# Kernel tuning notes

Hardware: AMD Instinct MI355X
Metric: run time of the kernel (lower is better)

## Reference

```python
import jax, jax.numpy as jnp
import numpy as np

N = 50000      # nodes
E = 1600000    # edges (before self loops)
IN = 128
OUT = 128
H = 4
HD = OUT // H  # head dim = 32


def setup_inputs() -> dict:
    key = jax.random.key(0)
    k1, k2, k3, k4, k5 = jax.random.split(key, 5)
    x = jax.random.normal(k1, (N, IN), dtype=jnp.float32)
    edge_index = jax.random.randint(k2, (2, E), 0, N, dtype=jnp.int64)
    # xavier-uniform-ish scales
    W = jax.random.normal(k3, (OUT, IN), dtype=jnp.float32) * (1.0 / np.sqrt(IN))
    att_src = jax.random.normal(k4, (1, H, HD), dtype=jnp.float32) * 0.1
    att_dst = jax.random.normal(k5, (1, H, HD), dtype=jnp.float32) * 0.1
    return {"x": x, "edge_index": edge_index, "W": W, "att_src": att_src, "att_dst": att_dst}


def reference(x, edge_index, W, att_src, att_dst):
    n = x.shape[0]
    # add self loops (tg.utils.add_self_loops appends [i, i] edges)
    loops = jnp.arange(n, dtype=edge_index.dtype)
    ei = jnp.concatenate([edge_index, jnp.stack([loops, loops])], axis=1)
    src, dst = ei[0], ei[1]

    # linear projection, split into heads: [n, H, HD]
    h = (x @ W.T).reshape(n, H, HD)

    # per-node attention logits per head: [n, H]
    a_src = jnp.sum(h * att_src, axis=-1)
    a_dst = jnp.sum(h * att_dst, axis=-1)

    # per-edge attention score: gather + leaky_relu
    alpha = a_src[src] + a_dst[dst]                      # [Etot, H]
    alpha = jax.nn.leaky_relu(alpha, negative_slope=0.2)

    # segment softmax grouped by destination node (numerically stable)
    m = jax.ops.segment_max(alpha, dst, num_segments=n)  # [n, H]
    e = jnp.exp(alpha - m[dst])
    s = jax.ops.segment_sum(e, dst, num_segments=n)      # [n, H]
    e = e / s[dst]                                       # [Etot, H]

    # weighted scatter-add aggregation; f_additive adds 1 to the weights
    msg = h[src] * (e[:, :, None] + 1.0)                 # [Etot, H, HD]
    out = jax.ops.segment_sum(msg, dst, num_segments=n)  # [n, H, HD]
    return out.reshape(n, -1)
```

## Files before the change

kernel.cpp:

```cpp
#include <hip/hip_runtime.h>

#define N_NODES 50000
#define E_EDGES 1600000
#define ETOT    (E_EDGES + N_NODES)
#define DIN  128
#define DOUT 128
#define NH   4
#define HD   32

typedef unsigned short ushort_t;
typedef unsigned int uint_t;
typedef __attribute__((ext_vector_type(8))) short bfrag;
typedef __attribute__((ext_vector_type(4))) float ffrag;

__device__ __forceinline__ ushort_t f2bf(float f) {
  uint_t u = __float_as_uint(f);
  u += 0x7fffu + ((u >> 16) & 1u);
  return (ushort_t)(u >> 16);
}
__device__ __forceinline__ float bf_lo(uint_t u) {
  return __uint_as_float(u << 16);
}
__device__ __forceinline__ float bf_hi(uint_t u) {
  return __uint_as_float(u & 0xffff0000u);
}

#define BSZ   256
#define NBUCK ((N_NODES + BSZ - 1) / BSZ)
#define CAP   10240
#define EPB_A 8192
#define NBLK_A ((ETOT + EPB_A - 1) / EPB_A)
#define NCHUNK 13

__global__ __launch_bounds__(256, 4) void fused_binA_gemm_kernel(
    const int* __restrict__ ei, int* __restrict__ gcur,
    uint_t* __restrict__ ebuf,
    const float* __restrict__ x, const float* __restrict__ W,
    const float* __restrict__ att_src, const float* __restrict__ att_dst,
    ushort_t* __restrict__ hb, float* __restrict__ a_src,
    float* __restrict__ a_dst) {
  __shared__ int hist[NBUCK];
  __shared__ int base[NBUCK];
  __shared__ ushort_t Ws[DIN * DOUT];
  const int tid = threadIdx.x;

  if (blockIdx.x < NBLK_A) {
    const int e0 = blockIdx.x * EPB_A;
    const int e1 = min(e0 + EPB_A, ETOT);
    for (int i = tid; i < NBUCK; i += 256) hist[i] = 0;
    __syncthreads();
    for (int e = e0 + tid; e < e1; e += 256) {
      int di = (e < E_EDGES) ? ei[E_EDGES + e] : (e - E_EDGES);
      atomicAdd(&hist[di >> 8], 1);
    }
    __syncthreads();
    for (int i = tid; i < NBUCK; i += 256) {
      int c = hist[i];
      base[i] = (c > 0) ? (i * CAP + atomicAdd(&gcur[i], c)) : 0;
      hist[i] = 0;
    }
    __syncthreads();
    for (int e = e0 + tid; e < e1; e += 256) {
      int si, di;
      if (e < E_EDGES) { si = ei[e]; di = ei[E_EDGES + e]; }
      else             { si = e - E_EDGES; di = si; }
      int b = di >> 8;
      int pos = base[b] + atomicAdd(&hist[b], 1);
      if (pos < (b + 1) * CAP)
        ebuf[pos] = ((uint_t)(di & 255) << 24) | (uint_t)si;
    }
    return;
  }

  const int gb = blockIdx.x - NBLK_A;
  for (int u = tid; u < 2048; u += 256) {
    int row = u >> 4;
    float4 w0 = *(const float4*)&W[u * 8];
    float4 w1 = *(const float4*)&W[u * 8 + 4];
    uint4 pk;
    pk.x = (uint_t)f2bf(w0.x) | ((uint_t)f2bf(w0.y) << 16);
    pk.y = (uint_t)f2bf(w0.z) | ((uint_t)f2bf(w0.w) << 16);
    pk.z = (uint_t)f2bf(w1.x) | ((uint_t)f2bf(w1.y) << 16);
    pk.w = (uint_t)f2bf(w1.z) | ((uint_t)f2bf(w1.w) << 16);
    *(uint4*)&Ws[(u ^ (row & 7)) * 8] = pk;
  }
  __syncthreads();

  const int wv = tid >> 6, l = tid & 63;
  const int lr = l & 15, lg = l >> 4;
  const int nbase = gb * 64 + wv * 16;
  int na = nbase + lr;
  if (na >= N_NODES) na = N_NODES - 1;
  const float* xrow = x + (size_t)na * DIN;

  ffrag acc[8];
#pragma unroll
  for (int oc = 0; oc < 8; oc++) acc[oc] = (ffrag){0.f, 0.f, 0.f, 0.f};

#pragma unroll
  for (int kt = 0; kt < 4; kt++) {
    float4 x0 = *(const float4*)&xrow[kt * 32 + lg * 8];
    float4 x1 = *(const float4*)&xrow[kt * 32 + lg * 8 + 4];
    bfrag a;
    a[0] = (short)f2bf(x0.x); a[1] = (short)f2bf(x0.y);
    a[2] = (short)f2bf(x0.z); a[3] = (short)f2bf(x0.w);
    a[4] = (short)f2bf(x1.x); a[5] = (short)f2bf(x1.y);
    a[6] = (short)f2bf(x1.z); a[7] = (short)f2bf(x1.w);
#pragma unroll
    for (int oc = 0; oc < 8; oc++) {
      const int u = ((oc * 16 + lr) << 4) + kt * 4 + lg;
      const bfrag b = *(const bfrag*)&Ws[(u ^ (lr & 7)) * 8];
      acc[oc] = __builtin_amdgcn_mfma_f32_16x16x32_bf16(a, b, acc[oc], 0, 0, 0);
    }
  }

#pragma unroll
  for (int oc = 0; oc < 8; oc++) {
#pragma unroll
    for (int j = 0; j < 4; j++) {
      int n = nbase + lg * 4 + j;
      if (n < N_NODES)
        hb[((size_t)n << 7) + oc * 16 + lr] = f2bf(acc[oc][j]);
    }
  }

  float asv[8], adv[8];
#pragma unroll
  for (int oc = 0; oc < 8; oc++) {
    asv[oc] = att_src[oc * 16 + lr];
    adv[oc] = att_dst[oc * 16 + lr];
  }
#pragma unroll
  for (int j = 0; j < 4; j++) {
    float ps[4] = {0.f, 0.f, 0.f, 0.f};
    float pd[4] = {0.f, 0.f, 0.f, 0.f};
#pragma unroll
    for (int oc = 0; oc < 8; oc++) {
      ps[oc >> 1] = fmaf(acc[oc][j], asv[oc], ps[oc >> 1]);
      pd[oc >> 1] = fmaf(acc[oc][j], adv[oc], pd[oc >> 1]);
    }
#pragma unroll
    for (int off = 1; off < 16; off <<= 1) {
#pragma unroll
      for (int hd = 0; hd < 4; hd++) {
        ps[hd] += __shfl_xor(ps[hd], off);
        pd[hd] += __shfl_xor(pd[hd], off);
      }
    }
    int n = nbase + lg * 4 + j;
    if (n < N_NODES && lr < 4) {
      float vs = lr == 0 ? ps[0] : lr == 1 ? ps[1] : lr == 2 ? ps[2] : ps[3];
      float vd = lr == 0 ? pd[0] : lr == 1 ? pd[1] : lr == 2 ? pd[2] : pd[3];
      a_src[n * NH + lr] = vs;
      a_dst[n * NH + lr] = vd;
    }
  }
}

__global__ __launch_bounds__(256) void binB_kernel(
    const uint_t* __restrict__ ebuf, const int* __restrict__ gcur,
    int* __restrict__ rs, int* __restrict__ re, int* __restrict__ col) {
  __shared__ int cnt[BSZ * NCHUNK];
  __shared__ int roff[BSZ * NCHUNK];
  __shared__ int wsum2[4];
  const int b = blockIdx.x;
  const int tid = threadIdx.x;
  const int ln = tid & 63, wv = tid >> 6;
  const int n0 = b << 8;
  const int nn = min(BSZ, N_NODES - n0);
  const int s0 = b * CAP;
  const int s1 = s0 + min(gcur[b], CAP);
  for (int k = tid; k < BSZ * NCHUNK; k += 256) cnt[k] = 0;
  __syncthreads();
  for (int i = s0 + tid; i < s1; i += 256) {
    uint_t p = ebuf[i];
    int key = (int)(p >> 24) * NCHUNK + (int)((p & 0xFFFFFFu) >> 12);
    atomicAdd(&cnt[key], 1);
  }
  __syncthreads();
  int pref[NCHUNK];
  int tot = 0;
#pragma unroll
  for (int k = 0; k < NCHUNK; k++) { pref[k] = tot; tot += cnt[tid * NCHUNK + k]; }
  int xx = tot;
#pragma unroll
  for (int off = 1; off < 64; off <<= 1) {
    int y = __shfl_up(xx, off, 64);
    if (ln >= off) xx += y;
  }
  if (ln == 63) wsum2[wv] = xx;
  __syncthreads();
  if (tid < 4) {
    int w = wsum2[tid];
#pragma unroll
    for (int off = 1; off < 4; off <<= 1) {
      int y = __shfl_up(w, off, 64);
      if (tid >= off) w += y;
    }
    wsum2[tid] = w;
  }
  __syncthreads();
  int wo = (wv == 0) ? 0 : wsum2[wv - 1];
  const int nodebase = xx + wo - tot;
#pragma unroll
  for (int k = 0; k < NCHUNK; k++) roff[tid * NCHUNK + k] = nodebase + pref[k];
  if (tid < nn) {
    rs[n0 + tid] = s0 + nodebase;
    re[n0 + tid] = s0 + nodebase + tot;
  }
  __syncthreads();
  for (int k = tid; k < BSZ * NCHUNK; k += 256) cnt[k] = 0;
  __syncthreads();
  for (int i = s0 + tid; i < s1; i += 256) {
    uint_t p = ebuf[i];
    int si = (int)(p & 0xFFFFFFu);
    int key = (int)(p >> 24) * NCHUNK + (si >> 12);
    int pos = atomicAdd(&cnt[key], 1);
    int q = s0 + roff[key] + pos;
    if (q >= 0 && q < NBUCK * CAP) col[q] = si;
  }
}

#define NPB 16
#define CH  16

__global__ __launch_bounds__(256, 8) void agg_kernel(
    const int* __restrict__ col, const int* __restrict__ rs,
    const int* __restrict__ re, const ushort_t* __restrict__ hb,
    const float* __restrict__ a_src, const float* __restrict__ a_dst,
    float* __restrict__ out) {
  __shared__ float w_lds[NPB][CH][NH];
  __shared__ int   si_lds[NPB][CH];
  const int tid  = threadIdx.x;
  const int slot = tid >> 4;
  const int t    = tid & 15;
  const int node = blockIdx.x * NPB + slot;
  const int start = rs[node];
  const int deg   = re[node] - start;
  const float4 ad = *(const float4*)(a_dst + (size_t)node * NH);

  float s0 = 0.f, s1 = 0.f, s2 = 0.f, s3 = 0.f;
  for (int j = t; j < deg; j += 16) {
    int si = col[start + j];
    si = si < N_NODES ? si : 0;
    float4 as = *(const float4*)(a_src + (size_t)si * NH);
    float v0 = as.x + ad.x; v0 = v0 > 0.f ? v0 : 0.2f * v0;
    float v1 = as.y + ad.y; v1 = v1 > 0.f ? v1 : 0.2f * v1;
    float v2 = as.z + ad.z; v2 = v2 > 0.f ? v2 : 0.2f * v2;
    float v3 = as.w + ad.w; v3 = v3 > 0.f ? v3 : 0.2f * v3;
    s0 += __expf(v0);
    s1 += __expf(v1);
    s2 += __expf(v2);
    s3 += __expf(v3);
  }
#pragma unroll
  for (int off = 1; off < 16; off <<= 1) {
    s0 += __shfl_xor(s0, off);
    s1 += __shfl_xor(s1, off);
    s2 += __shfl_xor(s2, off);
    s3 += __shfl_xor(s3, off);
  }
  const float i0 = 1.f / s0, i1 = 1.f / s1, i2 = 1.f / s2, i3 = 1.f / s3;

  const int head = t >> 2;
  const int c8 = t << 3;
  const ushort_t* hc = hb + c8;
  float a0 = 0.f, a1 = 0.f, a2 = 0.f, a3 = 0.f;
  float a4 = 0.f, a5 = 0.f, a6 = 0.f, a7 = 0.f;

  for (int base_e = 0; base_e < deg; base_e += CH) {
    int nch = deg - base_e;
    if (nch > CH) nch = CH;
    if (t < nch) {
      int si = col[start + base_e + t];
      si = si < N_NODES ? si : 0;
      si_lds[slot][t] = si;
      float4 as = *(const float4*)(a_src + (size_t)si * NH);
      float v0 = as.x + ad.x; v0 = v0 > 0.f ? v0 : 0.2f * v0;
      float v1 = as.y + ad.y; v1 = v1 > 0.f ? v1 : 0.2f * v1;
      float v2 = as.z + ad.z; v2 = v2 > 0.f ? v2 : 0.2f * v2;
      float v3 = as.w + ad.w; v3 = v3 > 0.f ? v3 : 0.2f * v3;
      w_lds[slot][t][0] = __expf(v0) * i0 + 1.f;
      w_lds[slot][t][1] = __expf(v1) * i1 + 1.f;
      w_lds[slot][t][2] = __expf(v2) * i2 + 1.f;
      w_lds[slot][t][3] = __expf(v3) * i3 + 1.f;
    }
    __builtin_amdgcn_fence(__ATOMIC_ACQ_REL, "wavefront");
#pragma unroll 4
    for (int j = 0; j < nch; j++) {
      int si = si_lds[slot][j];
      float w = w_lds[slot][j][head];
      const uint4 hv = *(const uint4*)(hc + ((size_t)si << 7));
      a0 = fmaf(bf_lo(hv.x), w, a0);
      a1 = fmaf(bf_hi(hv.x), w, a1);
      a2 = fmaf(bf_lo(hv.y), w, a2);
      a3 = fmaf(bf_hi(hv.y), w, a3);
      a4 = fmaf(bf_lo(hv.z), w, a4);
      a5 = fmaf(bf_hi(hv.z), w, a5);
      a6 = fmaf(bf_lo(hv.w), w, a6);
      a7 = fmaf(bf_hi(hv.w), w, a7);
    }
    __builtin_amdgcn_fence(__ATOMIC_ACQ_REL, "wavefront");
  }
  float* op = out + ((size_t)node << 7) + c8;
  *(float4*)(op)     = make_float4(a0, a1, a2, a3);
  *(float4*)(op + 4) = make_float4(a4, a5, a6, a7);
}

extern "C" void kernel_launch(void* const* d_in, const int* in_sizes, int n_in,
                              void* d_out, int out_size, void* d_ws, size_t ws_size,
                              hipStream_t stream) {
  const float* x       = (const float*)d_in[0];
  const int*   ei      = (const int*)d_in[1];
  const float* W       = (const float*)d_in[2];
  const float* att_src = (const float*)d_in[3];
  const float* att_dst = (const float*)d_in[4];
  float* out = (float*)d_out;

  ushort_t* hb = (ushort_t*)d_ws;
  float* a_src = (float*)(hb + (size_t)N_NODES * DOUT);
  float* a_dst = a_src + (size_t)N_NODES * NH;
  int* gcur    = (int*)(a_dst + (size_t)N_NODES * NH);
  int* rs      = gcur + NBUCK;
  int* re      = rs + N_NODES;
  int* col     = re + N_NODES;
  uint_t* ebuf = (uint_t*)(col + NBUCK * CAP);

  hipMemsetAsync(gcur, 0, (size_t)NBUCK * sizeof(int), stream);

  const int gemm_blocks = (N_NODES + 63) / 64;
  fused_binA_gemm_kernel<<<NBLK_A + gemm_blocks, 256, 0, stream>>>(
      ei, gcur, ebuf, x, W, att_src, att_dst, hb, a_src, a_dst);
  binB_kernel<<<NBUCK, 256, 0, stream>>>(ebuf, gcur, rs, re, col);
  agg_kernel<<<N_NODES / NPB, 256, 0, stream>>>(col, rs, re, hb, a_src, a_dst, out);
}
```

Baseline: 123.8 us.

## Fuse softmax normalization into single aggregation pass and shrink bucket size

The aggregation kernel no longer makes a separate pass over each node's edges to compute the softmax denominator. It accumulates unnormalized exp-weighted and plain sums together and applies 1/s at the end, which removes a second read of col and a_src per edge at the cost of eight more accumulator registers. Binning now uses 64-node buckets with smaller capacity and edges-per-block, so the prefix scan in binB fits in one wavefront with no cross-wave sync. The smaller buckets give more binB blocks and more global atomics in binA.

```diff
diff --git a/kernel.cpp b/kernel.cpp
--- a/kernel.cpp
+++ b/kernel.cpp
@@ -25,10 +25,10 @@
   return __uint_as_float(u & 0xffff0000u);
 }
 
-#define BSZ   256
+#define BSZ   64
 #define NBUCK ((N_NODES + BSZ - 1) / BSZ)
-#define CAP   10240
-#define EPB_A 8192
+#define CAP   2560
+#define EPB_A 4096
 #define NBLK_A ((ETOT + EPB_A - 1) / EPB_A)
 #define NCHUNK 13
 
@@ -51,7 +51,7 @@
     __syncthreads();
     for (int e = e0 + tid; e < e1; e += 256) {
       int di = (e < E_EDGES) ? ei[E_EDGES + e] : (e - E_EDGES);
-      atomicAdd(&hist[di >> 8], 1);
+      atomicAdd(&hist[di >> 6], 1);
     }
     __syncthreads();
     for (int i = tid; i < NBUCK; i += 256) {
@@ -64,10 +64,10 @@
       int si, di;
       if (e < E_EDGES) { si = ei[e]; di = ei[E_EDGES + e]; }
       else             { si = e - E_EDGES; di = si; }
-      int b = di >> 8;
+      int b = di >> 6;
       int pos = base[b] + atomicAdd(&hist[b], 1);
       if (pos < (b + 1) * CAP)
-        ebuf[pos] = ((uint_t)(di & 255) << 24) | (uint_t)si;
+        ebuf[pos] = ((uint_t)(di & 63) << 24) | (uint_t)si;
     }
     return;
   }
@@ -162,11 +162,9 @@
     int* __restrict__ rs, int* __restrict__ re, int* __restrict__ col) {
   __shared__ int cnt[BSZ * NCHUNK];
   __shared__ int roff[BSZ * NCHUNK];
-  __shared__ int wsum2[4];
   const int b = blockIdx.x;
   const int tid = threadIdx.x;
-  const int ln = tid & 63, wv = tid >> 6;
-  const int n0 = b << 8;
+  const int n0 = b << 6;
   const int nn = min(BSZ, N_NODES - n0);
   const int s0 = b * CAP;
   const int s1 = s0 + min(gcur[b], CAP);
@@ -178,35 +176,24 @@
     atomicAdd(&cnt[key], 1);
   }
   __syncthreads();
-  int pref[NCHUNK];
-  int tot = 0;
-#pragma unroll
-  for (int k = 0; k < NCHUNK; k++) { pref[k] = tot; tot += cnt[tid * NCHUNK + k]; }
-  int xx = tot;
-#pragma unroll
-  for (int off = 1; off < 64; off <<= 1) {
-    int y = __shfl_up(xx, off, 64);
-    if (ln >= off) xx += y;
-  }
-  if (ln == 63) wsum2[wv] = xx;
-  __syncthreads();
-  if (tid < 4) {
-    int w = wsum2[tid];
-#pragma unroll
-    for (int off = 1; off < 4; off <<= 1) {
-      int y = __shfl_up(w, off, 64);
-      if (tid >= off) w += y;
-    }
-    wsum2[tid] = w;
-  }
-  __syncthreads();
-  int wo = (wv == 0) ? 0 : wsum2[wv - 1];
-  const int nodebase = xx + wo - tot;
-#pragma unroll
-  for (int k = 0; k < NCHUNK; k++) roff[tid * NCHUNK + k] = nodebase + pref[k];
-  if (tid < nn) {
-    rs[n0 + tid] = s0 + nodebase;
-    re[n0 + tid] = s0 + nodebase + tot;
+  if (tid < BSZ) {
+    int pref[NCHUNK];
+    int tot = 0;
+#pragma unroll
+    for (int k = 0; k < NCHUNK; k++) { pref[k] = tot; tot += cnt[tid * NCHUNK + k]; }
+    int xx = tot;
+#pragma unroll
+    for (int off = 1; off < 64; off <<= 1) {
+      int y = __shfl_up(xx, off, 64);
+      if (tid >= off) xx += y;
+    }
+    const int nodebase = xx - tot;
+#pragma unroll
+    for (int k = 0; k < NCHUNK; k++) roff[tid * NCHUNK + k] = nodebase + pref[k];
+    if (tid < nn) {
+      rs[n0 + tid] = s0 + nodebase;
+      re[n0 + tid] = s0 + nodebase + tot;
+    }
   }
   __syncthreads();
   for (int k = tid; k < BSZ * NCHUNK; k += 256) cnt[k] = 0;
@@ -239,34 +226,14 @@
   const int deg   = re[node] - start;
   const float4 ad = *(const float4*)(a_dst + (size_t)node * NH);
 
-  float s0 = 0.f, s1 = 0.f, s2 = 0.f, s3 = 0.f;
-  for (int j = t; j < deg; j += 16) {
-    int si = col[start + j];
-    si = si < N_NODES ? si : 0;
-    float4 as = *(const float4*)(a_src + (size_t)si * NH);
-    float v0 = as.x + ad.x; v0 = v0 > 0.f ? v0 : 0.2f * v0;
-    float v1 = as.y + ad.y; v1 = v1 > 0.f ? v1 : 0.2f * v1;
-    float v2 = as.z + ad.z; v2 = v2 > 0.f ? v2 : 0.2f * v2;
-    float v3 = as.w + ad.w; v3 = v3 > 0.f ? v3 : 0.2f * v3;
-    s0 += __expf(v0);
-    s1 += __expf(v1);
-    s2 += __expf(v2);
-    s3 += __expf(v3);
-  }
-#pragma unroll
-  for (int off = 1; off < 16; off <<= 1) {
-    s0 += __shfl_xor(s0, off);
-    s1 += __shfl_xor(s1, off);
-    s2 += __shfl_xor(s2, off);
-    s3 += __shfl_xor(s3, off);
-  }
-  const float i0 = 1.f / s0, i1 = 1.f / s1, i2 = 1.f / s2, i3 = 1.f / s3;
-
   const int head = t >> 2;
   const int c8 = t << 3;
   const ushort_t* hc = hb + c8;
+  float s = 0.f;
   float a0 = 0.f, a1 = 0.f, a2 = 0.f, a3 = 0.f;
   float a4 = 0.f, a5 = 0.f, a6 = 0.f, a7 = 0.f;
+  float b0 = 0.f, b1 = 0.f, b2 = 0.f, b3 = 0.f;
+  float b4 = 0.f, b5 = 0.f, b6 = 0.f, b7 = 0.f;
 
   for (int base_e = 0; base_e < deg; base_e += CH) {
     int nch = deg - base_e;
@@ -280,31 +247,39 @@
       float v1 = as.y + ad.y; v1 = v1 > 0.f ? v1 : 0.2f * v1;
       float v2 = as.z + ad.z; v2 = v2 > 0.f ? v2 : 0.2f * v2;
       float v3 = as.w + ad.w; v3 = v3 > 0.f ? v3 : 0.2f * v3;
-      w_lds[slot][t][0] = __expf(v0) * i0 + 1.f;
-      w_lds[slot][t][1] = __expf(v1) * i1 + 1.f;
-      w_lds[slot][t][2] = __expf(v2) * i2 + 1.f;
-      w_lds[slot][t][3] = __expf(v3) * i3 + 1.f;
+      w_lds[slot][t][0] = __expf(v0);
+      w_lds[slot][t][1] = __expf(v1);
+      w_lds[slot][t][2] = __expf(v2);
+      w_lds[slot][t][3] = __expf(v3);
     }
     __builtin_amdgcn_fence(__ATOMIC_ACQ_REL, "wavefront");
-#pragma unroll 4
+#pragma unroll 2
     for (int j = 0; j < nch; j++) {
       int si = si_lds[slot][j];
-      float w = w_lds[slot][j][head];
+      float e = w_lds[slot][j][head];
+      s += e;
       const uint4 hv = *(const uint4*)(hc + ((size_t)si << 7));
-      a0 = fmaf(bf_lo(hv.x), w, a0);
-      a1 = fmaf(bf_hi(hv.x), w, a1);
-      a2 = fmaf(bf_lo(hv.y), w, a2);
-      a3 = fmaf(bf_hi(hv.y), w, a3);
-      a4 = fmaf(bf_lo(hv.z), w, a4);
-      a5 = fmaf(bf_hi(hv.z), w, a5);
-      a6 = fmaf(bf_lo(hv.w), w, a6);
-      a7 = fmaf(bf_hi(hv.w), w, a7);
+      float h0 = bf_lo(hv.x), h1 = bf_hi(hv.x);
+      float h2 = bf_lo(hv.y), h3 = bf_hi(hv.y);
+      float h4 = bf_lo(hv.z), h5 = bf_hi(hv.z);
+      float h6 = bf_lo(hv.w), h7 = bf_hi(hv.w);
+      a0 = fmaf(h0, e, a0); b0 += h0;
+      a1 = fmaf(h1, e, a1); b1 += h1;
+      a2 = fmaf(h2, e, a2); b2 += h2;
+      a3 = fmaf(h3, e, a3); b3 += h3;
+      a4 = fmaf(h4, e, a4); b4 += h4;
+      a5 = fmaf(h5, e, a5); b5 += h5;
+      a6 = fmaf(h6, e, a6); b6 += h6;
+      a7 = fmaf(h7, e, a7); b7 += h7;
     }
     __builtin_amdgcn_fence(__ATOMIC_ACQ_REL, "wavefront");
   }
+  const float inv = 1.0f / s;
   float* op = out + ((size_t)node << 7) + c8;
-  *(float4*)(op)     = make_float4(a0, a1, a2, a3);
-  *(float4*)(op + 4) = make_float4(a4, a5, a6, a7);
+  *(float4*)(op)     = make_float4(fmaf(a0, inv, b0), fmaf(a1, inv, b1),
+                                   fmaf(a2, inv, b2), fmaf(a3, inv, b3));
+  *(float4*)(op + 4) = make_float4(fmaf(a4, inv, b4), fmaf(a5, inv, b5),
+                                   fmaf(a6, inv, b6), fmaf(a7, inv, b7));
 }
 
 extern "C" void kernel_launch(void* const* d_in, const int* in_sizes, int n_in,
@@ -324,7 +299,7 @@
   int* rs      = gcur + NBUCK;
   int* re      = rs + N_NODES;
   int* col     = re + N_NODES;
-  uint_t* ebuf = (uint_t*)(col + NBUCK * CAP);
+  uint_t* ebuf = (uint_t*)(col + (size_t)NBUCK * CAP);
 
   hipMemsetAsync(gcur, 0, (size_t)NBUCK * sizeof(int), stream);
 
```

Measured after the change: 105.3 us. 15.0% less time.
